# Performance work log

Hardware: AMD Instinct MI355X
Metric: run time of the kernel (lower is better)

Reference implementation:

```python
import jax, jax.numpy as jnp
import numpy as np

D_MODEL = 1024
NUM_HEADS = 16
HEAD_DIM = D_MODEL // NUM_HEADS
MAX_SEQ_LEN = 2048
THETA = 10000.0
B, T = 2, 2048


def precompute_cos_sin(head_dim, max_len, theta):
    freqs = 1.0 / theta ** (jnp.arange(0, head_dim, 2, dtype=jnp.float32) / head_dim)
    t = jnp.arange(max_len, dtype=jnp.float32)
    f = jnp.outer(t, freqs)  # [max_len, head_dim//2]
    return jnp.concatenate([jnp.cos(f), jnp.sin(f)], axis=-1)  # [max_len, head_dim]


def apply_rotary_emb(x, cos_sin):
    # x: [B, H, T, Hs]; cos_sin: [T, Hs]
    xr = x.reshape(*x.shape[:-1], -1, 2)
    x1, x2 = xr[..., 0], xr[..., 1]
    cos, sin = jnp.split(cos_sin, 2, axis=-1)  # each [T, Hs//2]
    out = jnp.stack([x1 * cos - x2 * sin, x1 * sin + x2 * cos], axis=-1)
    return out.reshape(x.shape).astype(x.dtype)


def setup_inputs() -> dict:
    key = jax.random.key(0)
    ks = jax.random.split(key, 5)
    scale = 1.0 / np.sqrt(D_MODEL)
    return {
        'x': jax.random.normal(ks[0], (B, T, D_MODEL), dtype=jnp.float32),
        'wq': jax.random.normal(ks[1], (D_MODEL, D_MODEL), dtype=jnp.float32) * scale,
        'wk': jax.random.normal(ks[2], (D_MODEL, D_MODEL), dtype=jnp.float32) * scale,
        'wv': jax.random.normal(ks[3], (D_MODEL, D_MODEL), dtype=jnp.float32) * scale,
        'wo': jax.random.normal(ks[4], (D_MODEL, D_MODEL), dtype=jnp.float32) * scale,
    }


def reference(x, wq, wk, wv, wo):
    seq_len = x.shape[1]
    # Linear: einsum('...i,oi->...o'), weight stored as [out, in]
    q = jnp.einsum('bti,oi->bto', x, wq)
    k = jnp.einsum('bti,oi->bto', x, wk)
    v = jnp.einsum('bti,oi->bto', x, wv)
    # split heads: B T (nH Hs) -> B nH T Hs
    def split_heads(t):
        return t.reshape(t.shape[0], t.shape[1], NUM_HEADS, HEAD_DIM).transpose(0, 2, 1, 3)
    xq, xk, xv = split_heads(q), split_heads(k), split_heads(v)
    cos_sin = precompute_cos_sin(HEAD_DIM, MAX_SEQ_LEN, THETA)[:seq_len]
    xq = apply_rotary_emb(xq, cos_sin)
    xk = apply_rotary_emb(xk, cos_sin)
    scores = jnp.einsum('bhqd,bhkd->bhqk', xq, xk) / jnp.sqrt(jnp.float32(HEAD_DIM))
    causal = jnp.tril(jnp.ones((seq_len, seq_len), dtype=bool))
    scores = jnp.where(causal[None, None], scores, -jnp.inf)
    attn = jax.nn.softmax(scores, axis=-1)
    xo = jnp.einsum('bhqk,bhkd->bhqd', attn, xv)
    xo = xo.transpose(0, 2, 1, 3).reshape(x.shape[0], seq_len, D_MODEL)
    return jnp.einsum('bti,oi->bto', xo, wo)
```

## Files before the change

### kernel.cpp

```cpp
#include <hip/hip_runtime.h>
#include <hip/hip_bf16.h>

typedef __hip_bfloat16 bf16;
using s8v = __attribute__((ext_vector_type(8))) short;
using s4v = __attribute__((ext_vector_type(4))) short;
using f4v = __attribute__((ext_vector_type(4))) float;

#define D_MODEL 1024
#define NHEADS  16
#define HDIM    64
#define TSEQ    2048
#define NBATCH  2
#define BT      (NBATCH * TSEQ)

__device__ inline short f2bf_bits(float f) {
    bf16 h = __float2bfloat16(f);
    return *reinterpret_cast<short*>(&h);
}

__device__ inline void load8(const bf16* p, s8v& o) { o = *(const s8v*)p; }
__device__ inline void load8(const float* p, s8v& o) {
    const f4v a = *(const f4v*)p;
    const f4v b = *(const f4v*)(p + 4);
    s8v r;
    r[0] = f2bf_bits(a[0]); r[1] = f2bf_bits(a[1]);
    r[2] = f2bf_bits(a[2]); r[3] = f2bf_bits(a[3]);
    r[4] = f2bf_bits(b[0]); r[5] = f2bf_bits(b[1]);
    r[6] = f2bf_bits(b[2]); r[7] = f2bf_bits(b[3]);
    o = r;
}

__device__ inline void storeC(bf16* p, float v)  { *p = __float2bfloat16(v); }
__device__ inline void storeC(float* p, float v) { *p = v; }

__device__ inline void gload_lds16(const bf16* g, short* l) {
    __builtin_amdgcn_global_load_lds(
        (__attribute__((address_space(1))) void*)(unsigned long long)(size_t)g,
        (__attribute__((address_space(3))) void*)l,
        16, 0, 0);
}

__device__ inline void stage8(const bf16* g, short* l) { gload_lds16(g, l); }
__device__ inline void stage8(const float* g, short* l) {
    s8v v; load8(g, v); *(s8v*)l = v;
}

__global__ __launch_bounds__(256) void cvt_kernel(
    const float* __restrict__ src, bf16* __restrict__ dst)
{
    const size_t i = ((size_t)blockIdx.x * 256 + threadIdx.x) * 8;
    s8v v; load8(src + i, v);
    *(s8v*)&dst[i] = v;
}

template <typename TA, typename TW, typename TC>
__global__ __launch_bounds__(256, 2) void gemm_bt(
    const TA* __restrict__ A,
    const TW* __restrict__ W0, const TW* __restrict__ W1, const TW* __restrict__ W2,
    TC* __restrict__ C0, TC* __restrict__ C1, TC* __restrict__ C2,
    bf16* __restrict__ VT)
{
    const TW* W = (blockIdx.z == 0) ? W0 : (blockIdx.z == 1) ? W1 : W2;
    TC*       C = (blockIdx.z == 0) ? C0 : (blockIdx.z == 1) ? C1 : C2;
    const bool vt_mode = (VT != nullptr) && (blockIdx.z == 2);

    constexpr int K = 1024, N = 1024;
    __shared__ __align__(16) short As[128 * 64];
    __shared__ __align__(16) short Ws[128 * 64];

    const int t    = threadIdx.x;
    const int lane = t & 63;
    const int wave = t >> 6;
    const int m16  = lane & 15;
    const int quad = lane >> 4;
    const int wm   = (wave >> 1) * 64;
    const int wn   = (wave & 1) * 64;
    const int rowBase = blockIdx.x * 128;
    const int colBase = blockIdx.y * 128;

    f4v acc[4][4];
#pragma unroll
    for (int i = 0; i < 4; ++i)
#pragma unroll
        for (int j = 0; j < 4; ++j) acc[i][j] = f4v{0.f, 0.f, 0.f, 0.f};

    for (int kk = 0; kk < K / 64; ++kk) {
#pragma unroll
        for (int r = 0; r < 4; ++r) {
            const int chunk = r * 256 + t;
            const int row   = chunk >> 3;
            const int c8s   = (chunk & 7) ^ (row & 7);
            stage8(A + (size_t)(rowBase + row) * K + kk * 64 + c8s * 8, &As[chunk * 8]);
            stage8(W + (size_t)(colBase + row) * K + kk * 64 + c8s * 8, &Ws[chunk * 8]);
        }
        __syncthreads();

#pragma unroll
        for (int ks = 0; ks < 2; ++ks) {
            s8v af[4], bw[4];
#pragma unroll
            for (int mt = 0; mt < 4; ++mt) {
                const int rowa = wm + mt * 16 + m16;
                af[mt] = *(const s8v*)&As[rowa * 64 + ((ks * 4 + quad) ^ (rowa & 7)) * 8];
            }
#pragma unroll
            for (int nt = 0; nt < 4; ++nt) {
                const int roww = wn + nt * 16 + m16;
                bw[nt] = *(const s8v*)&Ws[roww * 64 + ((ks * 4 + quad) ^ (roww & 7)) * 8];
            }
#pragma unroll
            for (int mt = 0; mt < 4; ++mt)
#pragma unroll
                for (int nt = 0; nt < 4; ++nt)
                    acc[mt][nt] = __builtin_amdgcn_mfma_f32_16x16x32_bf16(
                        af[mt], bw[nt], acc[mt][nt], 0, 0, 0);
        }
        __syncthreads();
    }

    if (vt_mode) {
#pragma unroll
        for (int mt = 0; mt < 4; ++mt)
#pragma unroll
            for (int nt = 0; nt < 4; ++nt) {
                const int col  = colBase + wn + nt * 16 + m16;
                const int row0 = rowBase + wm + mt * 16 + quad * 4;
                const int bb   = row0 >> 11;
                const int tt   = row0 & (TSEQ - 1);
                s4v pk;
#pragma unroll
                for (int r = 0; r < 4; ++r) pk[r] = f2bf_bits(acc[mt][nt][r]);
                *(s4v*)&VT[((size_t)(bb * 1024 + col)) * TSEQ + tt] = pk;
            }
    } else {
#pragma unroll
        for (int mt = 0; mt < 4; ++mt)
#pragma unroll
            for (int nt = 0; nt < 4; ++nt)
#pragma unroll
                for (int r = 0; r < 4; ++r) {
                    const int row = rowBase + wm + mt * 16 + quad * 4 + r;
                    const int col = colBase + wn + nt * 16 + m16;
                    storeC(&C[(size_t)row * N + col], acc[mt][nt][r]);
                }
    }
}

__global__ __launch_bounds__(256) void rope_inplace(
    bf16* __restrict__ qp, bf16* __restrict__ kp)
{
    const int idx = blockIdx.x * 256 + threadIdx.x;
    const int i  = idx & 31;
    const int h  = (idx >> 5) & (NHEADS - 1);
    const int tt = (idx >> 9) & (TSEQ - 1);
    const int b  = idx >> 20;

    const size_t src = (size_t)(b * TSEQ + tt) * D_MODEL + h * HDIM + 2 * i;

    const float inv_freq = expf(-(float)i * (9.210340371976184f / 32.0f));
    const float f = (float)tt * inv_freq;
    float s, c;
    sincosf(f, &s, &c);

    const float q1 = __bfloat162float(qp[src]);
    const float q2 = __bfloat162float(qp[src + 1]);
    qp[src]     = __float2bfloat16((q1 * c - q2 * s) * 0.125f);
    qp[src + 1] = __float2bfloat16((q1 * s + q2 * c) * 0.125f);

    const float k1 = __bfloat162float(kp[src]);
    const float k2 = __bfloat162float(kp[src + 1]);
    kp[src]     = __float2bfloat16(k1 * c - k2 * s);
    kp[src + 1] = __float2bfloat16(k1 * s + k2 * c);
}

__global__ __launch_bounds__(256, 2) void attn_kernel(
    bf16* __restrict__ qp, const bf16* __restrict__ kp,
    const bf16* __restrict__ vt)
{
    const int hb = blockIdx.x & 31;
    const int ib = blockIdx.x >> 5;
    const int h  = hb & (NHEADS - 1);
    const int b  = hb >> 4;
    const int t    = threadIdx.x;
    const int lane = t & 63;
    const int wave = t >> 6;
    const int m16  = lane & 15;
    const int quad = lane >> 4;

    bf16*       Qb  = qp + (size_t)b * TSEQ * D_MODEL + h * HDIM;
    const bf16* Kb  = kp + (size_t)b * TSEQ * D_MODEL + h * HDIM;
    const bf16* Vtb = vt + ((size_t)b * 1024 + h * HDIM) * TSEQ;

    __shared__ __align__(16) short Klds[128 * 64];
    __shared__ __align__(16) short Vlds[64 * 128];
    __shared__ __align__(16) short P_lds[4][16][136];

    s8v ones;
#pragma unroll
    for (int j = 0; j < 8; ++j) ones[j] = (short)0x3F80;

#pragma unroll 1
    for (int pass = 0; pass < 2; ++pass) {
        const int bx = pass ? (31 - ib) : ib;
        const int q0 = bx * 64 + wave * 16;

        const s8v aq0 = *(const s8v*)&Qb[(size_t)(q0 + m16) * D_MODEL + quad * 8];
        const s8v aq1 = *(const s8v*)&Qb[(size_t)(q0 + m16) * D_MODEL + 32 + quad * 8];

        f4v o_acc[4];
#pragma unroll
        for (int nd = 0; nd < 4; ++nd) o_acc[nd] = f4v{0.f, 0.f, 0.f, 0.f};
        f4v o_l = f4v{0.f, 0.f, 0.f, 0.f};

        const int iters = (bx + 2) >> 1;
#pragma unroll 1
        for (int it = 0; it < iters; ++it) {
            const int kv0 = it * 128;

            __syncthreads();

#pragma unroll
            for (int r = 0; r < 4; ++r) {
                const int chunk = r * 256 + t;
                const int row   = chunk >> 3;
                const int c8s   = (chunk & 7) ^ (row & 7);
                gload_lds16(Kb + (size_t)(kv0 + row) * D_MODEL + c8s * 8,
                            &Klds[chunk * 8]);
            }
#pragma unroll
            for (int r = 0; r < 4; ++r) {
                const int chunk = r * 256 + t;
                const int row   = chunk >> 4;
                const int c16s  = (chunk & 15) ^ (row & 15);
                gload_lds16(Vtb + (size_t)row * TSEQ + kv0 + c16s * 8,
                            &Vlds[chunk * 8]);
            }
            __syncthreads();

            f4v s_acc[8];
#pragma unroll
            for (int nk = 0; nk < 8; ++nk) s_acc[nk] = f4v{0.f, 0.f, 0.f, 0.f};
#pragma unroll
            for (int nk = 0; nk < 8; ++nk) {
                const int rowk = nk * 16 + m16;
                const int sw   = m16 & 7;
                const s8v bk0 = *(const s8v*)&Klds[rowk * 64 + (quad ^ sw) * 8];
                const s8v bk1 = *(const s8v*)&Klds[rowk * 64 + ((4 + quad) ^ sw) * 8];
                s_acc[nk] = __builtin_amdgcn_mfma_f32_16x16x32_bf16(aq0, bk0, s_acc[nk], 0, 0, 0);
                s_acc[nk] = __builtin_amdgcn_mfma_f32_16x16x32_bf16(aq1, bk1, s_acc[nk], 0, 0, 0);
            }

            const bool diag = (it == iters - 1);
#pragma unroll
            for (int nk = 0; nk < 8; ++nk) {
                const int kv = kv0 + nk * 16 + m16;
#pragma unroll
                for (int r = 0; r < 4; ++r) {
                    float p = __expf(s_acc[nk][r] - 12.0f);
                    if (diag) {
                        const int qi = q0 + quad * 4 + r;
                        p = (kv <= qi) ? p : 0.0f;
                    }
                    P_lds[wave][quad * 4 + r][nk * 16 + m16] = f2bf_bits(p);
                }
            }
            asm volatile("s_waitcnt lgkmcnt(0)" ::: "memory");

#pragma unroll
            for (int kt = 0; kt < 4; ++kt) {
                const s8v ap = *(const s8v*)&P_lds[wave][m16][kt * 32 + quad * 8];
#pragma unroll
                for (int nd = 0; nd < 4; ++nd) {
                    const int rowv = nd * 16 + m16;
                    const s8v bv = *(const s8v*)&Vlds[rowv * 128
                                                      + ((kt * 4 + quad) ^ m16) * 8];
                    o_acc[nd] = __builtin_amdgcn_mfma_f32_16x16x32_bf16(
                        ap, bv, o_acc[nd], 0, 0, 0);
                }
                o_l = __builtin_amdgcn_mfma_f32_16x16x32_bf16(ap, ones, o_l, 0, 0, 0);
            }
        }

        float inv_l[4];
#pragma unroll
        for (int r = 0; r < 4; ++r) inv_l[r] = 1.0f / o_l[r];
#pragma unroll
        for (int nd = 0; nd < 4; ++nd)
#pragma unroll
            for (int r = 0; r < 4; ++r) {
                const int qi = q0 + quad * 4 + r;
                Qb[(size_t)qi * D_MODEL + nd * 16 + m16] =
                    __float2bfloat16(o_acc[nd][r] * inv_l[r]);
            }
    }
}

extern "C" void kernel_launch(void* const* d_in, const int* in_sizes, int n_in,
                              void* d_out, int out_size, void* d_ws, size_t ws_size,
                              hipStream_t stream) {
    const float* x  = (const float*)d_in[0];
    const float* wq = (const float*)d_in[1];
    const float* wk = (const float*)d_in[2];
    const float* wv = (const float*)d_in[3];
    const float* wo = (const float*)d_in[4];
    float* out = (float*)d_out;

    bf16* ws = (bf16*)d_ws;
    const size_t SZ  = (size_t)BT * D_MODEL;
    const size_t SZW = (size_t)D_MODEL * D_MODEL;
    bf16* qp  = ws + 0 * SZ;
    bf16* kp  = ws + 1 * SZ;
    bf16* vt  = (bf16*)d_out;
    bf16* xb  = (bf16*)(out + 2 * 1024 * 1024);

    cvt_kernel<<<dim3(2048), 256, 0, stream>>>(x, xb);

    if (ws_size >= (2 * SZ + 4 * SZW) * sizeof(bf16)) {
        bf16* wqb = ws + 2 * SZ + 0 * SZW;
        bf16* wkb = ws + 2 * SZ + 1 * SZW;
        bf16* wvb = ws + 2 * SZ + 2 * SZW;
        bf16* wob = ws + 2 * SZ + 3 * SZW;
        cvt_kernel<<<dim3(512), 256, 0, stream>>>(wq, wqb);
        cvt_kernel<<<dim3(512), 256, 0, stream>>>(wk, wkb);
        cvt_kernel<<<dim3(512), 256, 0, stream>>>(wv, wvb);
        cvt_kernel<<<dim3(512), 256, 0, stream>>>(wo, wob);

        gemm_bt<bf16, bf16, bf16><<<dim3(32, 8, 3), 256, 0, stream>>>(
            xb, wqb, wkb, wvb, qp, kp, qp , vt);
        rope_inplace<<<dim3(8192), 256, 0, stream>>>(qp, kp);
        attn_kernel<<<dim3(512), 256, 0, stream>>>(qp, kp, vt);
        gemm_bt<bf16, bf16, float><<<dim3(32, 8, 1), 256, 0, stream>>>(
            qp, wob, wob, wob, out, out, out, nullptr);
    } else {
        bf16* wob = kp;
        gemm_bt<bf16, float, bf16><<<dim3(32, 8, 3), 256, 0, stream>>>(
            xb, wq, wk, wv, qp, kp, qp , vt);
        rope_inplace<<<dim3(8192), 256, 0, stream>>>(qp, kp);
        attn_kernel<<<dim3(512), 256, 0, stream>>>(qp, kp, vt);
        cvt_kernel<<<dim3(512), 256, 0, stream>>>(wo, wob);
        gemm_bt<bf16, bf16, float><<<dim3(32, 8, 1), 256, 0, stream>>>(
            qp, wob, wob, wob, out, out, out, nullptr);
    }
}
```

Measured before the change: 185.8 us.

## Fuse input conversions, use exp2 softmax, and shrink output GEMM row tile

Merges the five fp32-to-bf16 conversion launches into one kernel, which removes launch overhead. Folds log2(e) into the Q scale and the fixed max bias into the score accumulator's initial value, so the softmax uses a raw exp2 and skips a subtract per element. Templates the GEMM on its row tile and uses 64-row tiles for the output projection, which doubles its block count on the many-CU device at some cost in weight reuse. The fixed bias stays equivalent to the old 12-unit offset in natural-log units.

```diff
diff --git a/kernel.cpp b/kernel.cpp
--- a/kernel.cpp
+++ b/kernel.cpp
@@ -12,6 +12,9 @@
 #define TSEQ    2048
 #define NBATCH  2
 #define BT      (NBATCH * TSEQ)
+
+#define QSCALE  0.180336880111f
+#define SBIAS  -17.3123404907f
 
 __device__ inline short f2bf_bits(float f) {
     bf16 h = __float2bfloat16(f);
@@ -53,7 +56,26 @@
     *(s8v*)&dst[i] = v;
 }
 
-template <typename TA, typename TW, typename TC>
+__global__ __launch_bounds__(256) void cvt_all_kernel(
+    const float* __restrict__ x,  bf16* __restrict__ xb,
+    const float* __restrict__ wq, bf16* __restrict__ wqb,
+    const float* __restrict__ wk, bf16* __restrict__ wkb,
+    const float* __restrict__ wv, bf16* __restrict__ wvb,
+    const float* __restrict__ wo, bf16* __restrict__ wob)
+{
+    const int blk = blockIdx.x;
+    const float* src; bf16* dst; int base;
+    if (blk < 2048)      { src = x;  dst = xb;  base = 0; }
+    else if (blk < 2560) { src = wq; dst = wqb; base = 2048; }
+    else if (blk < 3072) { src = wk; dst = wkb; base = 2560; }
+    else if (blk < 3584) { src = wv; dst = wvb; base = 3072; }
+    else                 { src = wo; dst = wob; base = 3584; }
+    const size_t i = ((size_t)(blk - base) * 256 + threadIdx.x) * 8;
+    s8v v; load8(src + i, v);
+    *(s8v*)&dst[i] = v;
+}
+
+template <int TM, typename TA, typename TW, typename TC>
 __global__ __launch_bounds__(256, 2) void gemm_bt(
     const TA* __restrict__ A,
     const TW* __restrict__ W0, const TW* __restrict__ W1, const TW* __restrict__ W2,
@@ -65,7 +87,8 @@
     const bool vt_mode = (VT != nullptr) && (blockIdx.z == 2);
 
     constexpr int K = 1024, N = 1024;
-    __shared__ __align__(16) short As[128 * 64];
+    constexpr int MT = TM / 32;
+    __shared__ __align__(16) short As[TM * 64];
     __shared__ __align__(16) short Ws[128 * 64];
 
     const int t    = threadIdx.x;
@@ -73,33 +96,39 @@
     const int wave = t >> 6;
     const int m16  = lane & 15;
     const int quad = lane >> 4;
-    const int wm   = (wave >> 1) * 64;
+    const int wm   = (wave >> 1) * (TM / 2);
     const int wn   = (wave & 1) * 64;
-    const int rowBase = blockIdx.x * 128;
+    const int rowBase = blockIdx.x * TM;
     const int colBase = blockIdx.y * 128;
 
-    f4v acc[4][4];
-#pragma unroll
-    for (int i = 0; i < 4; ++i)
+    f4v acc[MT][4];
+#pragma unroll
+    for (int i = 0; i < MT; ++i)
 #pragma unroll
         for (int j = 0; j < 4; ++j) acc[i][j] = f4v{0.f, 0.f, 0.f, 0.f};
 
     for (int kk = 0; kk < K / 64; ++kk) {
+#pragma unroll
+        for (int r = 0; r < TM / 32; ++r) {
+            const int chunk = r * 256 + t;
+            const int row   = chunk >> 3;
+            const int c8s   = (chunk & 7) ^ (row & 7);
+            stage8(A + (size_t)(rowBase + row) * K + kk * 64 + c8s * 8, &As[chunk * 8]);
+        }
 #pragma unroll
         for (int r = 0; r < 4; ++r) {
             const int chunk = r * 256 + t;
             const int row   = chunk >> 3;
             const int c8s   = (chunk & 7) ^ (row & 7);
-            stage8(A + (size_t)(rowBase + row) * K + kk * 64 + c8s * 8, &As[chunk * 8]);
             stage8(W + (size_t)(colBase + row) * K + kk * 64 + c8s * 8, &Ws[chunk * 8]);
         }
         __syncthreads();
 
 #pragma unroll
         for (int ks = 0; ks < 2; ++ks) {
-            s8v af[4], bw[4];
-#pragma unroll
-            for (int mt = 0; mt < 4; ++mt) {
+            s8v af[MT], bw[4];
+#pragma unroll
+            for (int mt = 0; mt < MT; ++mt) {
                 const int rowa = wm + mt * 16 + m16;
                 af[mt] = *(const s8v*)&As[rowa * 64 + ((ks * 4 + quad) ^ (rowa & 7)) * 8];
             }
@@ -109,7 +138,7 @@
                 bw[nt] = *(const s8v*)&Ws[roww * 64 + ((ks * 4 + quad) ^ (roww & 7)) * 8];
             }
 #pragma unroll
-            for (int mt = 0; mt < 4; ++mt)
+            for (int mt = 0; mt < MT; ++mt)
 #pragma unroll
                 for (int nt = 0; nt < 4; ++nt)
                     acc[mt][nt] = __builtin_amdgcn_mfma_f32_16x16x32_bf16(
@@ -120,7 +149,7 @@
 
     if (vt_mode) {
 #pragma unroll
-        for (int mt = 0; mt < 4; ++mt)
+        for (int mt = 0; mt < MT; ++mt)
 #pragma unroll
             for (int nt = 0; nt < 4; ++nt) {
                 const int col  = colBase + wn + nt * 16 + m16;
@@ -134,7 +163,7 @@
             }
     } else {
 #pragma unroll
-        for (int mt = 0; mt < 4; ++mt)
+        for (int mt = 0; mt < MT; ++mt)
 #pragma unroll
             for (int nt = 0; nt < 4; ++nt)
 #pragma unroll
@@ -164,8 +193,8 @@
 
     const float q1 = __bfloat162float(qp[src]);
     const float q2 = __bfloat162float(qp[src + 1]);
-    qp[src]     = __float2bfloat16((q1 * c - q2 * s) * 0.125f);
-    qp[src + 1] = __float2bfloat16((q1 * s + q2 * c) * 0.125f);
+    qp[src]     = __float2bfloat16((q1 * c - q2 * s) * QSCALE);
+    qp[src + 1] = __float2bfloat16((q1 * s + q2 * c) * QSCALE);
 
     const float k1 = __bfloat162float(kp[src]);
     const float k2 = __bfloat162float(kp[src + 1]);
@@ -239,7 +268,8 @@
 
             f4v s_acc[8];
 #pragma unroll
-            for (int nk = 0; nk < 8; ++nk) s_acc[nk] = f4v{0.f, 0.f, 0.f, 0.f};
+            for (int nk = 0; nk < 8; ++nk)
+                s_acc[nk] = f4v{SBIAS, SBIAS, SBIAS, SBIAS};
 #pragma unroll
             for (int nk = 0; nk < 8; ++nk) {
                 const int rowk = nk * 16 + m16;
@@ -256,7 +286,7 @@
                 const int kv = kv0 + nk * 16 + m16;
 #pragma unroll
                 for (int r = 0; r < 4; ++r) {
-                    float p = __expf(s_acc[nk][r] - 12.0f);
+                    float p = __builtin_amdgcn_exp2f(s_acc[nk][r]);
                     if (diag) {
                         const int qi = q0 + quad * 4 + r;
                         p = (kv <= qi) ? p : 0.0f;
@@ -313,32 +343,29 @@
     bf16* vt  = (bf16*)d_out;
     bf16* xb  = (bf16*)(out + 2 * 1024 * 1024);
 
-    cvt_kernel<<<dim3(2048), 256, 0, stream>>>(x, xb);
-
     if (ws_size >= (2 * SZ + 4 * SZW) * sizeof(bf16)) {
         bf16* wqb = ws + 2 * SZ + 0 * SZW;
         bf16* wkb = ws + 2 * SZ + 1 * SZW;
         bf16* wvb = ws + 2 * SZ + 2 * SZW;
         bf16* wob = ws + 2 * SZ + 3 * SZW;
-        cvt_kernel<<<dim3(512), 256, 0, stream>>>(wq, wqb);
-        cvt_kernel<<<dim3(512), 256, 0, stream>>>(wk, wkb);
-        cvt_kernel<<<dim3(512), 256, 0, stream>>>(wv, wvb);
-        cvt_kernel<<<dim3(512), 256, 0, stream>>>(wo, wob);
-
-        gemm_bt<bf16, bf16, bf16><<<dim3(32, 8, 3), 256, 0, stream>>>(
+
+        cvt_all_kernel<<<dim3(4096), 256, 0, stream>>>(
+            x, xb, wq, wqb, wk, wkb, wv, wvb, wo, wob);
+        gemm_bt<128, bf16, bf16, bf16><<<dim3(32, 8, 3), 256, 0, stream>>>(
             xb, wqb, wkb, wvb, qp, kp, qp , vt);
         rope_inplace<<<dim3(8192), 256, 0, stream>>>(qp, kp);
         attn_kernel<<<dim3(512), 256, 0, stream>>>(qp, kp, vt);
-        gemm_bt<bf16, bf16, float><<<dim3(32, 8, 1), 256, 0, stream>>>(
+        gemm_bt<64, bf16, bf16, float><<<dim3(64, 8, 1), 256, 0, stream>>>(
             qp, wob, wob, wob, out, out, out, nullptr);
     } else {
         bf16* wob = kp;
-        gemm_bt<bf16, float, bf16><<<dim3(32, 8, 3), 256, 0, stream>>>(
+        cvt_kernel<<<dim3(2048), 256, 0, stream>>>(x, xb);
+        gemm_bt<128, bf16, float, bf16><<<dim3(32, 8, 3), 256, 0, stream>>>(
             xb, wq, wk, wv, qp, kp, qp , vt);
         rope_inplace<<<dim3(8192), 256, 0, stream>>>(qp, kp);
         attn_kernel<<<dim3(512), 256, 0, stream>>>(qp, kp, vt);
         cvt_kernel<<<dim3(512), 256, 0, stream>>>(wo, wob);
-        gemm_bt<bf16, bf16, float><<<dim3(32, 8, 1), 256, 0, stream>>>(
+        gemm_bt<64, bf16, bf16, float><<<dim3(64, 8, 1), 256, 0, stream>>>(
             qp, wob, wob, wob, out, out, out, nullptr);
     }
 }
```

Result: faster. 172.4 us (-7.2%).
